# Kernel optimization log

Hardware: AMD Instinct MI355X
Metric: run time of the kernel (lower is better)

## Reference

```python
import jax, jax.numpy as jnp
import numpy as np

B, S, D = 2, 1024, 1024
E, K, F, FS = 8, 2, 512, 1024

def setup_inputs() -> dict:
    key = jax.random.key(0)
    ks = jax.random.split(key, 9)
    s = lambda k, shape, fan: jax.random.normal(k, shape, jnp.float32) * (fan ** -0.5)
    return {
        "x": jax.random.normal(ks[0], (B, S, D), jnp.float32),
        "Wr": s(ks[1], (D, E), D),
        "Wg": s(ks[2], (E, D, F), D),
        "Wu": s(ks[3], (E, D, F), D),
        "Wd": s(ks[4], (E, F, D), F),
        "Sg": s(ks[5], (D, FS), D),
        "Su": s(ks[6], (D, FS), D),
        "Sd": s(ks[7], (FS, D), FS),
        "expert_bias": jnp.zeros((E,), jnp.float32),
    }

def reference(x, Wr, Wg, Wu, Wd, Sg, Su, Sd, expert_bias):
    b, s, d = x.shape
    xf = x.reshape(-1, d)                              # [T, D]
    T = xf.shape[0]
    logits = xf @ Wr + expert_bias                     # [T, E]
    top_v, top_i = jax.lax.top_k(logits, K)            # [T, K]
    probs = jax.nn.softmax(top_v, axis=-1)             # [T, K]
    # dense routing-weight matrix: zero for non-selected experts
    rw = jnp.zeros_like(logits).at[jnp.arange(T)[:, None], top_i].set(probs)  # [T, E]
    # SwiGLU experts, computed densely; routing weight zeros out unselected
    gate = jnp.einsum('td,edf->tef', xf, Wg)           # [T, E, F]
    up = jnp.einsum('td,edf->tef', xf, Wu)
    h = jax.nn.silu(gate) * up
    eo = jnp.einsum('tef,efd->ted', h, Wd)             # [T, E, D]
    out = jnp.einsum('te,ted->td', rw, eo)             # [T, D]
    # shared expert applied to all tokens
    out = out + (jax.nn.silu(xf @ Sg) * (xf @ Su)) @ Sd
    return out.reshape(b, s, d)
```

## Files before the change

### kernel.cpp

```cpp
#include <hip/hip_runtime.h>
#include <cstdint>
#include <cstddef>

typedef __attribute__((ext_vector_type(8))) short bf16x8;
typedef __attribute__((ext_vector_type(4))) float f32x4;
typedef __attribute__((ext_vector_type(4))) unsigned short u16x4;

#define AS1 __attribute__((address_space(1)))
#define AS3 __attribute__((address_space(3)))

__device__ __forceinline__ unsigned short f2bf(float f) {
  union { float f; unsigned int u; } v; v.f = f;
  unsigned int r = v.u + 0x7fffu + ((v.u >> 16) & 1u);
  return (unsigned short)(r >> 16);
}

__device__ __forceinline__ void gll16(const unsigned short* g, unsigned short* l) {
  __builtin_amdgcn_global_load_lds((const AS1 void*)g, (AS3 void*)l, 16, 0, 0);
}

__global__ __launch_bounds__(256) void cvt_bf16_kernel(const float* __restrict__ src,
                                                       unsigned short* __restrict__ dst, int n) {
  int idx = (blockIdx.x * blockDim.x + threadIdx.x) * 4;
  if (idx >= n) return;
  const float* s = src + idx;
  u16x4 o = { f2bf(s[0]), f2bf(s[1]), f2bf(s[2]), f2bf(s[3]) };
  *(u16x4*)(dst + idx) = o;
}

__global__ __launch_bounds__(256) void transpose_cvt_all(
    const float* __restrict__ Wg, const float* __restrict__ Wu,
    const float* __restrict__ Wd, const float* __restrict__ Sg,
    const float* __restrict__ Su, const float* __restrict__ Sd,
    unsigned short* __restrict__ WguT, unsigned short* __restrict__ WdT,
    unsigned short* __restrict__ SguT, unsigned short* __restrict__ SdT) {
  const int z = blockIdx.z;
  const float* src; unsigned short* dst; int R, C, drp;
  if (z < 8)       { src = Wg + (size_t)z * 524288; dst = WguT + (size_t)z * 1048576; R = 1024; C = 512; drp = 2048; }
  else if (z < 16) { src = Wu + (size_t)(z - 8) * 524288; dst = WguT + (size_t)(z - 8) * 1048576 + 1024; R = 1024; C = 512; drp = 2048; }
  else if (z < 24) { src = Wd + (size_t)(z - 16) * 524288; dst = WdT + (size_t)(z - 16) * 524288; R = 512; C = 1024; drp = 512; }
  else if (z == 24){ src = Sg; dst = SguT; R = 1024; C = 1024; drp = 2048; }
  else if (z == 25){ src = Su; dst = SguT + 1024; R = 1024; C = 1024; drp = 2048; }
  else             { src = Sd; dst = SdT; R = 1024; C = 1024; drp = 1024; }
  const int c0 = blockIdx.x * 64, r0 = blockIdx.y * 64;
  if (c0 >= C || r0 >= R) return;
  __shared__ float tile[64][65];
  const int tc = threadIdx.x & 63, tr = threadIdx.x >> 6;
#pragma unroll
  for (int i = 0; i < 16; i++) {
    int r = tr + i * 4;
    tile[r][tc] = src[(size_t)(r0 + r) * C + c0 + tc];
  }
  __syncthreads();
#pragma unroll
  for (int i = 0; i < 16; i++) {
    int cc = tr + i * 4;
    dst[(size_t)(c0 + cc) * drp + (r0 + tc)] = f2bf(tile[tc][cc]);
  }
}

__global__ __launch_bounds__(256) void logits_kernel(const float* __restrict__ x,
                                                     const float* __restrict__ Wr,
                                                     float* __restrict__ logits) {
  const int t = blockIdx.x * 4 + (threadIdx.x >> 6);
  const int lane = threadIdx.x & 63;
  const float* xr = x + (size_t)t * 1024;
  float acc[8];
#pragma unroll
  for (int e = 0; e < 8; e++) acc[e] = 0.f;
#pragma unroll
  for (int i = 0; i < 16; i++) {
    int d = lane + i * 64;
    float xv = xr[d];
    const float4* w = (const float4*)(Wr + d * 8);
    float4 w0 = w[0], w1 = w[1];
    acc[0] += xv * w0.x; acc[1] += xv * w0.y; acc[2] += xv * w0.z; acc[3] += xv * w0.w;
    acc[4] += xv * w1.x; acc[5] += xv * w1.y; acc[6] += xv * w1.z; acc[7] += xv * w1.w;
  }
#pragma unroll
  for (int off = 32; off > 0; off >>= 1)
#pragma unroll
    for (int e = 0; e < 8; e++) acc[e] += __shfl_down(acc[e], off);
  if (lane == 0) {
#pragma unroll
    for (int e = 0; e < 8; e++) logits[t * 8 + e] = acc[e];
  }
}

__global__ __launch_bounds__(1024) void assign_kernel(
    const float* __restrict__ logits, const float* __restrict__ bias,
    int* __restrict__ list, int* __restrict__ ridx, float* __restrict__ rp,
    int* __restrict__ counts_g, int* __restrict__ offs_g) {
  __shared__ int cnt[8];
  __shared__ int offs[9];
  const int tid = threadIdx.x;
  if (tid < 8) cnt[tid] = 0;
  __syncthreads();
  int te[2][2], tpos[2][2];
  float tp[2][2];
#pragma unroll
  for (int it = 0; it < 2; it++) {
    int t = tid + it * 1024;
    float v[8];
#pragma unroll
    for (int e = 0; e < 8; e++) v[e] = logits[t * 8 + e] + bias[e];
    int i0 = 0;
#pragma unroll
    for (int e = 1; e < 8; e++) if (v[e] > v[i0]) i0 = e;
    int i1 = (i0 == 0) ? 1 : 0;
#pragma unroll
    for (int e = 0; e < 8; e++) if (e != i0 && v[e] > v[i1]) i1 = e;
    float pa = 1.f / (1.f + __expf(v[i1] - v[i0]));
    te[it][0] = i0; te[it][1] = i1;
    tp[it][0] = pa; tp[it][1] = 1.f - pa;
    tpos[it][0] = atomicAdd(&cnt[i0], 1);
    tpos[it][1] = atomicAdd(&cnt[i1], 1);
  }
  __syncthreads();
  if (tid == 0) {
    int s = 0;
#pragma unroll
    for (int e = 0; e < 8; e++) { offs[e] = s; s += cnt[e]; }
    offs[8] = s;
#pragma unroll
    for (int e = 0; e < 8; e++) { counts_g[e] = cnt[e]; offs_g[e] = offs[e]; }
    offs_g[8] = s;
  }
  __syncthreads();
#pragma unroll
  for (int it = 0; it < 2; it++) {
    int t = tid + it * 1024;
#pragma unroll
    for (int k = 0; k < 2; k++) {
      int grow = offs[te[it][k]] + tpos[it][k];
      list[grow] = t;
      ridx[t * 2 + k] = grow;
      rp[t * 2 + k] = tp[it][k];
    }
  }
}

template <int NK>
__device__ __forceinline__ void kloop(
    const unsigned short* ga0, const unsigned short* ga1,
    const unsigned short* gb0, const unsigned short* gb1,
    unsigned short* lwA0, unsigned short* lwA1,
    unsigned short* lwB0, unsigned short* lwB1,
    const unsigned short* lrA, const unsigned short* lrB,
    f32x4 (&acc)[4][4]) {
  gll16(ga0, lwA0);          gll16(ga1, lwA1);
  gll16(gb0, lwB0);          gll16(gb1, lwB1);
  gll16(ga0 + 32, lwA0 + 4096); gll16(ga1 + 32, lwA1 + 4096);
  gll16(gb0 + 32, lwB0 + 4096); gll16(gb1 + 32, lwB1 + 4096);
#pragma unroll
  for (int i = 0; i < NK; ++i) {
    if (i + 1 < NK) asm volatile("s_waitcnt vmcnt(4) lgkmcnt(0)\n\ts_barrier" ::: "memory");
    else            asm volatile("s_waitcnt vmcnt(0) lgkmcnt(0)\n\ts_barrier" ::: "memory");
    if (i + 2 < NK) {
      const int bo = ((i + 2) % 3) * 4096;
      const int ko = (i + 2) * 32;
      gll16(ga0 + ko, lwA0 + bo); gll16(ga1 + ko, lwA1 + bo);
      gll16(gb0 + ko, lwB0 + bo); gll16(gb1 + ko, lwB1 + bo);
    }
    const int ro = (i % 3) * 4096;
    bf16x8 af[4], bf[4];
#pragma unroll
    for (int u = 0; u < 4; ++u) af[u] = *(const bf16x8*)(lrA + ro + u * 512);
#pragma unroll
    for (int u = 0; u < 4; ++u) bf[u] = *(const bf16x8*)(lrB + ro + u * 512);
#pragma unroll
    for (int ii = 0; ii < 4; ++ii)
#pragma unroll
      for (int jj = 0; jj < 4; ++jj)
        acc[ii][jj] = __builtin_amdgcn_mfma_f32_16x16x32_bf16(af[ii], bf[jj], acc[ii][jj], 0, 0, 0);
  }
}

template <int MODE>
__global__ __launch_bounds__(256, 2) void gemm_tn_kernel(
    const unsigned short* __restrict__ Xb, const unsigned short* __restrict__ He,
    const unsigned short* __restrict__ Hs, const unsigned short* __restrict__ Wgu,
    const unsigned short* __restrict__ Sgu, const unsigned short* __restrict__ Wd,
    const unsigned short* __restrict__ Sd, unsigned short* __restrict__ HeOut,
    unsigned short* __restrict__ HsOut, float* __restrict__ De, float* __restrict__ Ds,
    const int* __restrict__ list, const int* __restrict__ counts,
    const int* __restrict__ offs) {
  const int ez = blockIdx.z;
  int cnt, lda, K;
  const unsigned short* A;
  const unsigned short* B;
  const int* alist = nullptr;
  unsigned short* H = nullptr;
  float* D = nullptr;
  int ldh = 0;

  if (MODE == 0) {
    if (ez < 8) {
      if (blockIdx.y >= 8) return;
      cnt = counts[ez]; A = Xb; alist = list + offs[ez]; lda = 1024; K = 1024;
      B = Wgu + (size_t)ez * 1024 * 1024; H = HeOut + (size_t)offs[ez] * 512; ldh = 512;
    } else {
      cnt = 2048; A = Xb; lda = 1024; K = 1024; B = Sgu; H = HsOut; ldh = 1024;
    }
  } else {
    if (ez < 8) {
      cnt = counts[ez]; A = He + (size_t)offs[ez] * 512; lda = 512; K = 512;
      B = Wd + (size_t)ez * 1024 * 512; D = De + (size_t)offs[ez] * 1024;
    } else {
      cnt = 2048; A = Hs; lda = 1024; K = 1024; B = Sd; D = Ds;
    }
  }

  const int m0 = blockIdx.x * 128;
  if (m0 >= cnt) return;
  const int n0 = blockIdx.y * 128;

  __shared__ unsigned short As[3 * 4096];
  __shared__ unsigned short Bs[3 * 4096];

  const int tid = threadIdx.x;
  const int srow = tid >> 2;
  const int scol = (tid & 3) * 8;
  const int wuni = (tid >> 6) * 512;

  int r0 = m0 + srow; if (r0 >= cnt) r0 = cnt - 1;
  int r1 = m0 + srow + 64; if (r1 >= cnt) r1 = cnt - 1;
  size_t abase0, abase1;
  if (MODE == 0 && ez < 8) {
    abase0 = (size_t)alist[r0] * lda; abase1 = (size_t)alist[r1] * lda;
  } else {
    abase0 = (size_t)r0 * lda; abase1 = (size_t)r1 * lda;
  }

  const unsigned short* ga0 = A + abase0 + scol;
  const unsigned short* ga1 = A + abase1 + scol;
  const unsigned short* gb0 = B + (size_t)(n0 + srow) * K + scol;
  const unsigned short* gb1 = B + (size_t)(n0 + srow + 64) * K + scol;

  unsigned short* lwA0 = As + wuni;
  unsigned short* lwA1 = As + 2048 + wuni;
  unsigned short* lwB0 = Bs + wuni;
  unsigned short* lwB1 = Bs + 2048 + wuni;

  const int wave = tid >> 6;
  const int lane = tid & 63;
  const int wm = (wave & 1) * 64;
  const int wn = (wave >> 1) * 64;
  const int fl = lane & 15;
  const int q = lane >> 4;

  const unsigned short* lrA = As + (wm + fl) * 32 + q * 8;
  const unsigned short* lrB = Bs + (wn + fl) * 32 + q * 8;

  f32x4 acc[4][4];
  f32x4 zero = {0.f, 0.f, 0.f, 0.f};
#pragma unroll
  for (int i = 0; i < 4; i++)
#pragma unroll
    for (int j = 0; j < 4; j++) acc[i][j] = zero;

  if (MODE == 1 && ez < 8) kloop<16>(ga0, ga1, gb0, gb1, lwA0, lwA1, lwB0, lwB1, lrA, lrB, acc);
  else                     kloop<32>(ga0, ga1, gb0, gb1, lwA0, lwA1, lwB0, lwB1, lrA, lrB, acc);

  if (MODE == 0) {
#pragma unroll
    for (int i = 0; i < 4; i++) {
#pragma unroll
      for (int j = 0; j < 4; j++) {
#pragma unroll
        for (int r = 0; r < 4; r++) {
          int grow = m0 + wm + i * 16 + q * 4 + r;
          float v = acc[i][j][r];
          float pv = __shfl_xor(v, 1);
          if ((lane & 1) == 0 && grow < cnt) {
            float s = v / (1.f + __expf(-v));
            int colh = (n0 + wn + j * 16 + fl) >> 1;
            H[(size_t)grow * ldh + colh] = f2bf(s * pv);
          }
        }
      }
    }
  } else {
#pragma unroll
    for (int i = 0; i < 4; i++) {
#pragma unroll
      for (int r = 0; r < 4; r++) {
        int grow = m0 + wm + i * 16 + q * 4 + r;
        if (grow >= cnt) continue;
#pragma unroll
        for (int j = 0; j < 4; j++) {
          int col = n0 + wn + j * 16 + fl;
          D[(size_t)grow * 1024 + col] = acc[i][j][r];
        }
      }
    }
  }
}

__global__ __launch_bounds__(256) void combine_kernel(
    const float* __restrict__ Ds, const float* __restrict__ De,
    const int* __restrict__ ridx, const float* __restrict__ rp,
    float* __restrict__ out) {
  const int t = blockIdx.x;
  const int i0 = ridx[t * 2], i1 = ridx[t * 2 + 1];
  const float p0 = rp[t * 2], p1 = rp[t * 2 + 1];
  const float4* a  = (const float4*)(Ds + (size_t)t * 1024);
  const float4* b0 = (const float4*)(De + (size_t)i0 * 1024);
  const float4* b1 = (const float4*)(De + (size_t)i1 * 1024);
  float4* o = (float4*)(out + (size_t)t * 1024);
  int c = threadIdx.x;
  float4 va = a[c], v0 = b0[c], v1 = b1[c];
  float4 r;
  r.x = va.x + p0 * v0.x + p1 * v1.x;
  r.y = va.y + p0 * v0.y + p1 * v1.y;
  r.z = va.z + p0 * v0.z + p1 * v1.z;
  r.w = va.w + p0 * v0.w + p1 * v1.w;
  o[c] = r;
}

extern "C" void kernel_launch(void* const* d_in, const int* in_sizes, int n_in,
                              void* d_out, int out_size, void* d_ws, size_t ws_size,
                              hipStream_t stream) {
  const float* x    = (const float*)d_in[0];
  const float* Wr   = (const float*)d_in[1];
  const float* Wg   = (const float*)d_in[2];
  const float* Wu   = (const float*)d_in[3];
  const float* Wd   = (const float*)d_in[4];
  const float* Sg   = (const float*)d_in[5];
  const float* Su   = (const float*)d_in[6];
  const float* Sd   = (const float*)d_in[7];
  const float* bias = (const float*)d_in[8];
  float* out = (float*)d_out;

  char* ws = (char*)d_ws;
  size_t o = 0;
  auto alloc = [&](size_t b) { char* p = ws + o; o += (b + 255) & ~(size_t)255; return p; };
  unsigned short* Xb   = (unsigned short*)alloc((size_t)2048 * 1024 * 2);
  unsigned short* WguT = (unsigned short*)alloc((size_t)8 * 1024 * 1024 * 2);
  unsigned short* WdT  = (unsigned short*)alloc((size_t)8 * 1024 * 512 * 2);
  unsigned short* SguT = (unsigned short*)alloc((size_t)2048 * 1024 * 2);
  unsigned short* SdT  = (unsigned short*)alloc((size_t)1024 * 1024 * 2);
  float* logits = (float*)alloc((size_t)2048 * 8 * 4);
  int*   list   = (int*)alloc((size_t)4096 * 4);
  int*   ridx   = (int*)alloc((size_t)2048 * 2 * 4);
  float* rp     = (float*)alloc((size_t)2048 * 2 * 4);
  int*   counts = (int*)alloc(64);
  int*   offs   = (int*)alloc(64);
  unsigned short* He = (unsigned short*)alloc((size_t)4096 * 512 * 2);
  unsigned short* Hs = (unsigned short*)alloc((size_t)2048 * 1024 * 2);
  float* De = (float*)alloc((size_t)4096 * 1024 * 4);
  float* Ds = (float*)alloc((size_t)2048 * 1024 * 4);

  cvt_bf16_kernel<<<2048, 256, 0, stream>>>(x, Xb, 2048 * 1024);
  transpose_cvt_all<<<dim3(16, 16, 27), 256, 0, stream>>>(Wg, Wu, Wd, Sg, Su, Sd,
                                                          WguT, WdT, SguT, SdT);

  logits_kernel<<<512, 256, 0, stream>>>(x, Wr, logits);
  assign_kernel<<<1, 1024, 0, stream>>>(logits, bias, list, ridx, rp, counts, offs);

  gemm_tn_kernel<0><<<dim3(16, 16, 9), 256, 0, stream>>>(
      Xb, He, Hs, WguT, SguT, WdT, SdT, He, Hs, De, Ds, list, counts, offs);
  gemm_tn_kernel<1><<<dim3(16, 8, 9), 256, 0, stream>>>(
      Xb, He, Hs, WguT, SguT, WdT, SdT, He, Hs, De, Ds, list, counts, offs);

  combine_kernel<<<2048, 256, 0, stream>>>(Ds, De, ridx, rp, out);
}
```

Before: 239.3 us.

## Fuse x conversion into transpose kernel, vectorize transpose, reorder GEMM grid

Folds the x fp32→bf16 conversion into the weight transpose launch as extra z-slices, which removes one kernel launch. The transpose now reads float4 rows and writes 8-wide bf16 vectors instead of scalar accesses. The grouped GEMM grid is reordered so the expert index is blockIdx.x, which changes dispatch order and should spread the uneven expert work across CUs. The launch-bounds occupancy hint also goes from 2 to 3 blocks, which may constrain registers and cause spills.

```diff
diff --git a/kernel.cpp b/kernel.cpp
--- a/kernel.cpp
+++ b/kernel.cpp
@@ -19,22 +19,27 @@
   __builtin_amdgcn_global_load_lds((const AS1 void*)g, (AS3 void*)l, 16, 0, 0);
 }
 
-__global__ __launch_bounds__(256) void cvt_bf16_kernel(const float* __restrict__ src,
-                                                       unsigned short* __restrict__ dst, int n) {
-  int idx = (blockIdx.x * blockDim.x + threadIdx.x) * 4;
-  if (idx >= n) return;
-  const float* s = src + idx;
-  u16x4 o = { f2bf(s[0]), f2bf(s[1]), f2bf(s[2]), f2bf(s[3]) };
-  *(u16x4*)(dst + idx) = o;
-}
-
 __global__ __launch_bounds__(256) void transpose_cvt_all(
     const float* __restrict__ Wg, const float* __restrict__ Wu,
     const float* __restrict__ Wd, const float* __restrict__ Sg,
     const float* __restrict__ Su, const float* __restrict__ Sd,
+    const float* __restrict__ x,
     unsigned short* __restrict__ WguT, unsigned short* __restrict__ WdT,
-    unsigned short* __restrict__ SguT, unsigned short* __restrict__ SdT) {
+    unsigned short* __restrict__ SguT, unsigned short* __restrict__ SdT,
+    unsigned short* __restrict__ Xb) {
   const int z = blockIdx.z;
+  const int tid = threadIdx.x;
+
+  if (z >= 27) {
+    size_t off = (size_t)(z - 27) * 524288 + blockIdx.y * 32768 + blockIdx.x * 2048 + tid * 8;
+    const float4* s = (const float4*)(x + off);
+    float4 a = s[0], b = s[1];
+    bf16x8 o = { (short)f2bf(a.x), (short)f2bf(a.y), (short)f2bf(a.z), (short)f2bf(a.w),
+                 (short)f2bf(b.x), (short)f2bf(b.y), (short)f2bf(b.z), (short)f2bf(b.w) };
+    *(bf16x8*)(Xb + off) = o;
+    return;
+  }
+
   const float* src; unsigned short* dst; int R, C, drp;
   if (z < 8)       { src = Wg + (size_t)z * 524288; dst = WguT + (size_t)z * 1048576; R = 1024; C = 512; drp = 2048; }
   else if (z < 16) { src = Wu + (size_t)(z - 8) * 524288; dst = WguT + (size_t)(z - 8) * 1048576 + 1024; R = 1024; C = 512; drp = 2048; }
@@ -44,18 +49,27 @@
   else             { src = Sd; dst = SdT; R = 1024; C = 1024; drp = 1024; }
   const int c0 = blockIdx.x * 64, r0 = blockIdx.y * 64;
   if (c0 >= C || r0 >= R) return;
+
   __shared__ float tile[64][65];
-  const int tc = threadIdx.x & 63, tr = threadIdx.x >> 6;
-#pragma unroll
-  for (int i = 0; i < 16; i++) {
-    int r = tr + i * 4;
-    tile[r][tc] = src[(size_t)(r0 + r) * C + c0 + tc];
+  {
+    const int row = tid >> 2, cs = (tid & 3) * 16;
+    const float* sp = src + (size_t)(r0 + row) * C + c0 + cs;
+#pragma unroll
+    for (int k = 0; k < 4; k++) {
+      float4 v = ((const float4*)sp)[k];
+      tile[row][cs + k * 4 + 0] = v.x; tile[row][cs + k * 4 + 1] = v.y;
+      tile[row][cs + k * 4 + 2] = v.z; tile[row][cs + k * 4 + 3] = v.w;
+    }
   }
   __syncthreads();
 #pragma unroll
-  for (int i = 0; i < 16; i++) {
-    int cc = tr + i * 4;
-    dst[(size_t)(c0 + cc) * drp + (r0 + tc)] = f2bf(tile[tc][cc]);
+  for (int i = 0; i < 2; i++) {
+    const int cc = i * 32 + (tid >> 3);
+    const int rseg = (tid & 7) * 8;
+    bf16x8 o;
+#pragma unroll
+    for (int j = 0; j < 8; j++) o[j] = (short)f2bf(tile[rseg + j][cc]);
+    *(bf16x8*)(dst + (size_t)(c0 + cc) * drp + r0 + rseg) = o;
   }
 }
 
@@ -177,7 +191,7 @@
 }
 
 template <int MODE>
-__global__ __launch_bounds__(256, 2) void gemm_tn_kernel(
+__global__ __launch_bounds__(256, 3) void gemm_tn_kernel(
     const unsigned short* __restrict__ Xb, const unsigned short* __restrict__ He,
     const unsigned short* __restrict__ Hs, const unsigned short* __restrict__ Wgu,
     const unsigned short* __restrict__ Sgu, const unsigned short* __restrict__ Wd,
@@ -185,7 +199,7 @@
     unsigned short* __restrict__ HsOut, float* __restrict__ De, float* __restrict__ Ds,
     const int* __restrict__ list, const int* __restrict__ counts,
     const int* __restrict__ offs) {
-  const int ez = blockIdx.z;
+  const int ez = blockIdx.x;
   int cnt, lda, K;
   const unsigned short* A;
   const unsigned short* B;
@@ -196,7 +210,7 @@
 
   if (MODE == 0) {
     if (ez < 8) {
-      if (blockIdx.y >= 8) return;
+      if (blockIdx.z >= 8) return;
       cnt = counts[ez]; A = Xb; alist = list + offs[ez]; lda = 1024; K = 1024;
       B = Wgu + (size_t)ez * 1024 * 1024; H = HeOut + (size_t)offs[ez] * 512; ldh = 512;
     } else {
@@ -211,9 +225,9 @@
     }
   }
 
-  const int m0 = blockIdx.x * 128;
+  const int m0 = blockIdx.y * 128;
   if (m0 >= cnt) return;
-  const int n0 = blockIdx.y * 128;
+  const int n0 = blockIdx.z * 128;
 
   __shared__ unsigned short As[3 * 4096];
   __shared__ unsigned short Bs[3 * 4096];
@@ -351,16 +365,15 @@
   float* De = (float*)alloc((size_t)4096 * 1024 * 4);
   float* Ds = (float*)alloc((size_t)2048 * 1024 * 4);
 
-  cvt_bf16_kernel<<<2048, 256, 0, stream>>>(x, Xb, 2048 * 1024);
-  transpose_cvt_all<<<dim3(16, 16, 27), 256, 0, stream>>>(Wg, Wu, Wd, Sg, Su, Sd,
-                                                          WguT, WdT, SguT, SdT);
+  transpose_cvt_all<<<dim3(16, 16, 31), 256, 0, stream>>>(Wg, Wu, Wd, Sg, Su, Sd, x,
+                                                          WguT, WdT, SguT, SdT, Xb);
 
   logits_kernel<<<512, 256, 0, stream>>>(x, Wr, logits);
   assign_kernel<<<1, 1024, 0, stream>>>(logits, bias, list, ridx, rp, counts, offs);
 
-  gemm_tn_kernel<0><<<dim3(16, 16, 9), 256, 0, stream>>>(
+  gemm_tn_kernel<0><<<dim3(9, 16, 16), 256, 0, stream>>>(
       Xb, He, Hs, WguT, SguT, WdT, SdT, He, Hs, De, Ds, list, counts, offs);
-  gemm_tn_kernel<1><<<dim3(16, 8, 9), 256, 0, stream>>>(
+  gemm_tn_kernel<1><<<dim3(9, 16, 8), 256, 0, stream>>>(
       Xb, He, Hs, WguT, SguT, WdT, SdT, He, Hs, De, Ds, list, counts, offs);
 
   combine_kernel<<<2048, 256, 0, stream>>>(Ds, De, ridx, rp, out);
```

Measured after the change: 200.8 us. 1.19x faster.
